# Optimization experiments

Hardware: AMD Instinct MI355X
Metric: run time of the kernel (lower is better)

The kernel has to match this reference:

```python
import jax, jax.numpy as jnp
import numpy as np

B, N, C = 8, 1024, 768
H = 12
DH = C // H  # 64
FF = 3072
EPS = 1e-5


def _layer_norm(x, gamma, beta):
    mu = jnp.mean(x, axis=-1, keepdims=True)
    var = jnp.mean(jnp.square(x - mu), axis=-1, keepdims=True)
    return (x - mu) * jax.lax.rsqrt(var + EPS) * gamma + beta


def setup_inputs() -> dict:
    key = jax.random.key(0)
    ks = jax.random.split(key, 16)
    s_in = 1.0 / np.sqrt(C)
    s_ff = 1.0 / np.sqrt(FF)
    return {
        "x": jax.random.normal(ks[0], (B, N, C), dtype=jnp.float32),
        "Wq": jax.random.uniform(ks[1], (C, C), jnp.float32, -s_in, s_in),
        "bq": jax.random.uniform(ks[2], (C,), jnp.float32, -s_in, s_in),
        "Wk": jax.random.uniform(ks[3], (C, C), jnp.float32, -s_in, s_in),
        "bk": jax.random.uniform(ks[4], (C,), jnp.float32, -s_in, s_in),
        "Wv": jax.random.uniform(ks[5], (C, C), jnp.float32, -s_in, s_in),
        "bv": jax.random.uniform(ks[6], (C,), jnp.float32, -s_in, s_in),
        "Wo": jax.random.uniform(ks[7], (C, C), jnp.float32, -s_in, s_in),
        "bo": jax.random.uniform(ks[8], (C,), jnp.float32, -s_in, s_in),
        "g1": jnp.ones((C,), jnp.float32),
        "b1": jnp.zeros((C,), jnp.float32),
        "g2": jnp.ones((C,), jnp.float32),
        "b2": jnp.zeros((C,), jnp.float32),
        "W1": jax.random.uniform(ks[9], (C, FF), jnp.float32, -s_in, s_in),
        "bf1": jax.random.uniform(ks[10], (FF,), jnp.float32, -s_in, s_in),
        "W2": jax.random.uniform(ks[11], (FF, C), jnp.float32, -s_ff, s_ff),
        "bf2": jax.random.uniform(ks[12], (C,), jnp.float32, -s_ff, s_ff),
    }


def reference(x, Wq, bq, Wk, bk, Wv, bv, Wo, bo, g1, b1, g2, b2, W1, bf1, W2, bf2):
    # Pre-norm attention block
    xn = _layer_norm(x, g1, b1)
    q = (xn @ Wq + bq).reshape(B, N, H, DH)
    k = (xn @ Wk + bk).reshape(B, N, H, DH)
    v = (xn @ Wv + bv).reshape(B, N, H, DH)
    scores = jnp.einsum("bqhd,bkhd->bhqk", q, k) / np.sqrt(DH)  # [B,H,N,N]
    attn = jax.nn.softmax(scores, axis=-1)
    z = jnp.einsum("bhqk,bkhd->bqhd", attn, v).reshape(B, N, C)
    attn_out = z @ Wo + bo
    b = x + attn_out  # dropout is identity (p=0 / eval)
    # Pre-norm MLP block
    bn = _layer_norm(b, g2, b2)
    h = jax.nn.relu(bn @ W1 + bf1)
    y = b + (h @ W2 + bf2)
    return y
```

## Files before the change

### kernel.cpp

```cpp
#include <hip/hip_runtime.h>
#include <hip/hip_bf16.h>

#define BDIM 8
#define SEQ  1024
#define CH   768
#define NHD  12
#define DHD  64
#define FFD  3072
#define MR   (BDIM*SEQ)

typedef __attribute__((ext_vector_type(8))) short bf16x8;
typedef __attribute__((ext_vector_type(4))) float f32x4;
typedef unsigned int   u32;
typedef unsigned short u16;

__device__ __forceinline__ u16 f2bfu(float x) {
  __hip_bfloat16 h = __float2bfloat16(x);
  return *reinterpret_cast<u16*>(&h);
}

__device__ __forceinline__ void glds16(const void* g, void* l) {
  __builtin_amdgcn_global_load_lds(
      (const __attribute__((address_space(1))) u32*)g,
      (__attribute__((address_space(3))) u32*)l, 16, 0, 0);
}

__global__ __launch_bounds__(256) void k_transpose_all(
    const float* __restrict__ Wq, const float* __restrict__ Wk,
    const float* __restrict__ Wv, const float* __restrict__ Wo,
    const float* __restrict__ W1, const float* __restrict__ W2,
    u16* __restrict__ ws, const float* __restrict__ bq,
    const float* __restrict__ bk, const float* __restrict__ bv,
    float* __restrict__ bdst) {
  __shared__ float tile[32][33];
  int b = blockIdx.x;
  if (b >= 6912) {
    int i = (b - 6912) * 256 + threadIdx.x;
    if (i < 3 * CH)
      bdst[i] = i < CH ? bq[i] : (i < 2 * CH ? bk[i - CH] : bv[i - 2 * CH]);
    return;
  }
  int id, tb;
  if (b < 2304)      { id = b / 576; tb = b % 576; }
  else if (b < 4608) { id = 4;       tb = b - 2304; }
  else               { id = 5;       tb = b - 4608; }
  const float* src;
  u16* dst;
  int K, Nc;
  switch (id) {
    case 0: src = Wq; dst = ws;                      K = CH;  Nc = CH;  break;
    case 1: src = Wk; dst = ws + (size_t)CH*CH;      K = CH;  Nc = CH;  break;
    case 2: src = Wv; dst = ws + (size_t)2*CH*CH;    K = CH;  Nc = CH;  break;
    case 3: src = Wo; dst = ws + (size_t)3*CH*CH;    K = CH;  Nc = CH;  break;
    case 4: src = W1; dst = ws + (size_t)4*CH*CH;    K = CH;  Nc = FFD; break;
    default:src = W2; dst = ws + (size_t)4*CH*CH + (size_t)CH*FFD;
                                                     K = FFD; Nc = CH;  break;
  }
  int tilesx = Nc >> 5;
  int bx = (tb % tilesx) * 32;
  int by = (tb / tilesx) * 32;
  int tx = threadIdx.x & 31, ty = threadIdx.x >> 5;
#pragma unroll
  for (int j = 0; j < 32; j += 8)
    tile[ty + j][tx] = src[(size_t)(by + ty + j) * Nc + bx + tx];
  __syncthreads();
#pragma unroll
  for (int j = 0; j < 32; j += 8)
    dst[(size_t)(bx + ty + j) * K + by + tx] = f2bfu(tile[tx][ty + j]);
}

__global__ __launch_bounds__(256) void k_layernorm_bf16(
    const float* __restrict__ src, const float* __restrict__ gamma,
    const float* __restrict__ beta, u16* __restrict__ dst) {
  int row  = blockIdx.x * 4 + (threadIdx.x >> 6);
  int lane = threadIdx.x & 63;
  const float4* p4 = (const float4*)(src + (size_t)row * CH);
  float4 v[3];
  float s = 0.f, s2 = 0.f;
#pragma unroll
  for (int k = 0; k < 3; k++) {
    v[k] = p4[lane + k * 64];
    s  += v[k].x + v[k].y + v[k].z + v[k].w;
    s2 += v[k].x * v[k].x + v[k].y * v[k].y + v[k].z * v[k].z + v[k].w * v[k].w;
  }
#pragma unroll
  for (int m = 1; m < 64; m <<= 1) {
    s  += __shfl_xor(s,  m, 64);
    s2 += __shfl_xor(s2, m, 64);
  }
  float mean = s * (1.f / CH);
  float var  = s2 * (1.f / CH) - mean * mean;
  float rs   = rsqrtf(var + 1e-5f);
  u16* drow = dst + (size_t)row * CH;
#pragma unroll
  for (int k = 0; k < 3; k++) {
    int col = lane * 4 + k * 256;
    float4 gq = ((const float4*)gamma)[lane + k * 64];
    float4 bq = ((const float4*)beta )[lane + k * 64];
    u32 lo = (u32)f2bfu((v[k].x - mean) * rs * gq.x + bq.x) |
             ((u32)f2bfu((v[k].y - mean) * rs * gq.y + bq.y) << 16);
    u32 hi = (u32)f2bfu((v[k].z - mean) * rs * gq.z + bq.z) |
             ((u32)f2bfu((v[k].w - mean) * rs * gq.w + bq.w) << 16);
    uint2 w; w.x = lo; w.y = hi;
    *(uint2*)(drow + col) = w;
  }
}

enum { EPI_QKV = 0, EPI_RESID = 1, EPI_RELU = 2 };

template <int EPI>
__device__ __forceinline__ void gemm_epi(const f32x4& a, int row0, int col,
                                         float bval, const float* resid,
                                         void* outp, int Nmat) {
  if constexpr (EPI == EPI_QKV) {
    int sel = col / CH;
    int c = col - sel * CH;
    int h = c >> 6, d = c & 63;
    int bb = row0 >> 10, nn0 = row0 & (SEQ - 1);
    if (sel == 2) {
      union { uint2 u; u16 h4[4]; } pk;
#pragma unroll
      for (int r = 0; r < 4; r++) pk.h4[r] = f2bfu(a[r] + bval);
      *(uint2*)&((u16*)outp)[(size_t)2 * MR * CH +
                             (((size_t)(bb * NHD + h)) * DHD + d) * SEQ + nn0] =
          pk.u;
    } else {
#pragma unroll
      for (int r = 0; r < 4; r++)
        ((u16*)outp)[(size_t)sel * MR * CH +
                     (((size_t)(bb * NHD + h)) * SEQ + nn0 + r) * DHD + d] =
            f2bfu(a[r] + bval);
    }
  } else if constexpr (EPI == EPI_RESID) {
#pragma unroll
    for (int r = 0; r < 4; r++) {
      size_t idx = (size_t)(row0 + r) * Nmat + col;
      ((float*)outp)[idx] = a[r] + bval + resid[idx];
    }
  } else {
#pragma unroll
    for (int r = 0; r < 4; r++) {
      float val = a[r] + bval;
      ((u16*)outp)[(size_t)(row0 + r) * Nmat + col] =
          f2bfu(val > 0.f ? val : 0.f);
    }
  }
}

template <int EPI, int TM = 128>
__global__ __launch_bounds__(256, 2) void k_gemm(
    const u16* __restrict__ A, const u16* __restrict__ Bt,
    const float* __restrict__ bias, const float* __restrict__ resid,
    void* __restrict__ outp, int K, int Nmat) {
  __shared__ u16 As[2][TM * 32];
  __shared__ u16 Bs[2][128 * 32];
  constexpr int MF = TM / 32;
  int tid = threadIdx.x;
  int bm = blockIdx.x, bn = blockIdx.y;
  int lane = tid & 63, wid = tid >> 6;
  int wr = (wid >> 1) * (TM / 2), wc = (wid & 1) * 64;
  int lrow = lane & 15, g = lane >> 4;

  const u16* Abase = A + (size_t)(bm * TM) * K;
  const u16* Bbase = Bt + (size_t)(bn * 128) * K;

  auto stage = [&](int buf, int k0) {
#pragma unroll
    for (int r = 0; r < TM / 64; r++) {
      int c = tid + r * 256;
      int row = c >> 2;
      int scol = ((c & 3) ^ ((row >> 1) & 3)) * 8;
      glds16(Abase + (size_t)row * K + k0 + scol, &As[buf][c * 8]);
    }
#pragma unroll
    for (int r = 0; r < 2; r++) {
      int c = tid + r * 256;
      int row = c >> 2;
      int scol = ((c & 3) ^ ((row >> 1) & 3)) * 8;
      glds16(Bbase + (size_t)row * K + k0 + scol, &Bs[buf][c * 8]);
    }
  };

  int xsl = (g ^ ((lrow >> 1) & 3)) * 8;

  f32x4 acc[MF][4];
#pragma unroll
  for (int m = 0; m < MF; m++)
#pragma unroll
    for (int n = 0; n < 4; n++) acc[m][n] = {0.f, 0.f, 0.f, 0.f};

  int nk = K >> 5;
  stage(0, 0);
  for (int kt = 0; kt < nk; ++kt) {
    int buf = kt & 1;
    __syncthreads();
    if (kt + 1 < nk) stage(buf ^ 1, (kt + 1) << 5);
    bf16x8 af[MF], bfr[4];
#pragma unroll
    for (int m = 0; m < MF; m++)
      af[m] = *(const bf16x8*)&As[buf][(wr + m * 16 + lrow) * 32 + xsl];
#pragma unroll
    for (int n = 0; n < 4; n++)
      bfr[n] = *(const bf16x8*)&Bs[buf][(wc + n * 16 + lrow) * 32 + xsl];
    __builtin_amdgcn_s_setprio(1);
#pragma unroll
    for (int m = 0; m < MF; m++)
#pragma unroll
      for (int n = 0; n < 4; n++)
        acc[m][n] = __builtin_amdgcn_mfma_f32_16x16x32_bf16(af[m], bfr[n],
                                                            acc[m][n], 0, 0, 0);
    __builtin_amdgcn_s_setprio(0);
  }

#pragma unroll
  for (int m = 0; m < MF; m++) {
    int row0 = bm * TM + wr + m * 16 + g * 4;
#pragma unroll
    for (int n = 0; n < 4; n++) {
      int col = bn * 128 + wc + n * 16 + lrow;
      gemm_epi<EPI>(acc[m][n], row0, col, bias[col], resid, outp, Nmat);
    }
  }
}

template <int EPI>
__global__ __launch_bounds__(256, 2) void k_gemmk64(
    const u16* __restrict__ A, const u16* __restrict__ Bt,
    const float* __restrict__ bias, const float* __restrict__ resid,
    void* __restrict__ outp, int K, int Nmat) {
  __shared__ u16 As[2][64 * 64];
  __shared__ u16 Bs[2][128 * 64];
  int tid = threadIdx.x;
  int bm = blockIdx.x, bn = blockIdx.y;
  int lane = tid & 63, wid = tid >> 6;
  int wr = (wid >> 1) * 32, wc = (wid & 1) * 64;
  int lrow = lane & 15, g = lane >> 4;

  const u16* Abase = A + (size_t)(bm * 64) * K;
  const u16* Bbase = Bt + (size_t)(bn * 128) * K;

  auto stage = [&](int buf, int k0) {
#pragma unroll
    for (int r = 0; r < 2; r++) {
      int u = tid + r * 256;
      int row = u >> 3, slot = u & 7;
      glds16(Abase + (size_t)row * K + k0 + ((slot ^ (row & 7)) << 3),
             &As[buf][u * 8]);
    }
#pragma unroll
    for (int r = 0; r < 4; r++) {
      int u = tid + r * 256;
      int row = u >> 3, slot = u & 7;
      glds16(Bbase + (size_t)row * K + k0 + ((slot ^ (row & 7)) << 3),
             &Bs[buf][u * 8]);
    }
  };

  int sx = lrow & 7;
  int x0 = (g ^ sx) * 8;
  int x1 = ((4 + g) ^ sx) * 8;

  f32x4 acc[2][4];
#pragma unroll
  for (int m = 0; m < 2; m++)
#pragma unroll
    for (int n = 0; n < 4; n++) acc[m][n] = {0.f, 0.f, 0.f, 0.f};

  int nk = K >> 6;
  stage(0, 0);
  for (int kt = 0; kt < nk; ++kt) {
    int buf = kt & 1;
    __syncthreads();
    if (kt + 1 < nk) stage(buf ^ 1, (kt + 1) << 6);
#pragma unroll
    for (int ks = 0; ks < 2; ks++) {
      int xs = ks ? x1 : x0;
      bf16x8 af[2], bfr[4];
#pragma unroll
      for (int m = 0; m < 2; m++)
        af[m] = *(const bf16x8*)&As[buf][(wr + m * 16 + lrow) * 64 + xs];
#pragma unroll
      for (int n = 0; n < 4; n++)
        bfr[n] = *(const bf16x8*)&Bs[buf][(wc + n * 16 + lrow) * 64 + xs];
      __builtin_amdgcn_s_setprio(1);
#pragma unroll
      for (int m = 0; m < 2; m++)
#pragma unroll
        for (int n = 0; n < 4; n++)
          acc[m][n] = __builtin_amdgcn_mfma_f32_16x16x32_bf16(
              af[m], bfr[n], acc[m][n], 0, 0, 0);
      __builtin_amdgcn_s_setprio(0);
    }
  }

#pragma unroll
  for (int m = 0; m < 2; m++) {
    int row0 = bm * 64 + wr + m * 16 + g * 4;
#pragma unroll
    for (int n = 0; n < 4; n++) {
      int col = bn * 128 + wc + n * 16 + lrow;
      gemm_epi<EPI>(acc[m][n], row0, col, bias[col], resid, outp, Nmat);
    }
  }
}

__global__ __launch_bounds__(512, 4) void k_attn(
    const u16* __restrict__ Q, const u16* __restrict__ Kk,
    const u16* __restrict__ Vt, u16* __restrict__ Z) {
  __shared__ u16 Ks[2][64 * 64];
  __shared__ u16 Vs[2][64 * 64];
  __shared__ u32 Psu[8][64 * 9];
  int tid = threadIdx.x, lane = tid & 63, wid = tid >> 6;
  int lrow = lane & 15, g = lane >> 4;
  int id  = blockIdx.x;
  int nid = (id & 7) * 96 + (id >> 3);
  int bh = nid >> 3;
  int qtile = (nid & 7) * 128;
  size_t base = (size_t)bh * SEQ * DHD;
  int bb = bh / NHD, hh = bh % NHD;
  int qrow0 = qtile + wid * 16;

  bf16x8 qf[2];
#pragma unroll
  for (int ks = 0; ks < 2; ks++)
    qf[ks] = *(const bf16x8*)(Q + base + (size_t)(qrow0 + lrow) * DHD +
                              ks * 32 + g * 8);

  f32x4 accO[4];
  float mrun = -1e30f, lrun = 0.f;
#pragma unroll
  for (int n = 0; n < 4; n++) accO[n] = {0.f, 0.f, 0.f, 0.f};

  int srow = tid >> 3;
  int swz  = (((tid & 7) * 16) ^ ((srow & 7) << 4)) >> 1;
  const u16* kg0 = Kk + base + (size_t)srow * DHD + swz;
  const u16* vg0 = Vt + base + (size_t)srow * SEQ + swz;

  auto stageKV = [&](int buf, int t) {
    glds16(kg0 + (size_t)t * 64 * DHD, &Ks[buf][tid * 8]);
    glds16(vg0 + t * 64,               &Vs[buf][tid * 8]);
  };

  int rc0 = ((g * 16)      ^ ((lrow & 7) << 4)) >> 1;
  int rc1 = ((64 + g * 16) ^ ((lrow & 7) << 4)) >> 1;

  stageKV(0, 0);
  for (int t = 0; t < 16; ++t) {
    int buf = t & 1;
    __syncthreads();
    if (t + 1 < 16) stageKV(buf ^ 1, t + 1);

    f32x4 sacc[4];
    __builtin_amdgcn_s_setprio(1);
#pragma unroll
    for (int n = 0; n < 4; n++) {
      bf16x8 kf0 = *(const bf16x8*)&Ks[buf][(n * 16 + lrow) * 64 + rc0];
      bf16x8 kf1 = *(const bf16x8*)&Ks[buf][(n * 16 + lrow) * 64 + rc1];
      sacc[n] = {0.f, 0.f, 0.f, 0.f};
      sacc[n] = __builtin_amdgcn_mfma_f32_16x16x32_bf16(kf0, qf[0], sacc[n], 0, 0, 0);
      sacc[n] = __builtin_amdgcn_mfma_f32_16x16x32_bf16(kf1, qf[1], sacc[n], 0, 0, 0);
    }
    __builtin_amdgcn_s_setprio(0);

    float mx = fmaxf(fmaxf(fmaxf(sacc[0][0], sacc[0][1]),
                           fmaxf(sacc[0][2], sacc[0][3])),
                     fmaxf(fmaxf(sacc[1][0], sacc[1][1]),
                           fmaxf(sacc[1][2], sacc[1][3])));
    mx = fmaxf(mx, fmaxf(fmaxf(fmaxf(sacc[2][0], sacc[2][1]),
                               fmaxf(sacc[2][2], sacc[2][3])),
                         fmaxf(fmaxf(sacc[3][0], sacc[3][1]),
                               fmaxf(sacc[3][2], sacc[3][3]))));
    mx *= 0.125f;
    mx = fmaxf(mx, __shfl_xor(mx, 16, 64));
    mx = fmaxf(mx, __shfl_xor(mx, 32, 64));

    if (__all(mx <= mrun + 8.f)) {
      float psum = 0.f;
#pragma unroll
      for (int n = 0; n < 4; n++)
#pragma unroll
        for (int r = 0; r < 4; r++) {
          float p = __expf(sacc[n][r] * 0.125f - mrun);
          sacc[n][r] = p;
          psum += p;
        }
      psum += __shfl_xor(psum, 16, 64);
      psum += __shfl_xor(psum, 32, 64);
      lrun += psum;
    } else {
      float mnew = fmaxf(mrun, mx);
      float alpha = __expf(mrun - mnew);
      float psum = 0.f;
#pragma unroll
      for (int n = 0; n < 4; n++)
#pragma unroll
        for (int r = 0; r < 4; r++) {
          float p = __expf(sacc[n][r] * 0.125f - mnew);
          sacc[n][r] = p;
          psum += p;
        }
      psum += __shfl_xor(psum, 16, 64);
      psum += __shfl_xor(psum, 32, 64);
      lrun = lrun * alpha + psum;
      mrun = mnew;
#pragma unroll
      for (int r = 0; r < 4; r++) {
        float ar = __shfl(alpha, (lane & 48) | (g * 4 + r), 64);
#pragma unroll
        for (int n = 0; n < 4; n++) accO[n][r] *= ar;
      }
    }

#pragma unroll
    for (int n = 0; n < 4; n++) {
      u32 lo = (u32)f2bfu(sacc[n][0]) | ((u32)f2bfu(sacc[n][1]) << 16);
      u32 hi = (u32)f2bfu(sacc[n][2]) | ((u32)f2bfu(sacc[n][3]) << 16);
      Psu[wid][lane * 9 + 2 * n]     = lo;
      Psu[wid][lane * 9 + 2 * n + 1] = hi;
    }

    int laneA = lrow + ((g & 1) << 5);
    int laneB = laneA + 16;
    int nsel = g >> 1;
    __builtin_amdgcn_s_setprio(1);
#pragma unroll
    for (int ks = 0; ks < 2; ks++) {
      int nks = 2 * ks + nsel;
      union { bf16x8 v; u32 w[4]; } pk;
      pk.w[0] = Psu[wid][laneA * 9 + 2 * nks];
      pk.w[1] = Psu[wid][laneA * 9 + 2 * nks + 1];
      pk.w[2] = Psu[wid][laneB * 9 + 2 * nks];
      pk.w[3] = Psu[wid][laneB * 9 + 2 * nks + 1];
      int rc = ks ? rc1 : rc0;
#pragma unroll
      for (int n = 0; n < 4; n++) {
        bf16x8 vf = *(const bf16x8*)&Vs[buf][(n * 16 + lrow) * 64 + rc];
        accO[n] = __builtin_amdgcn_mfma_f32_16x16x32_bf16(pk.v, vf,
                                                          accO[n], 0, 0, 0);
      }
    }
    __builtin_amdgcn_s_setprio(0);
  }

#pragma unroll
  for (int r = 0; r < 4; r++) {
    float lr = __shfl(lrun, (lane & 48) | (g * 4 + r), 64);
    float inv = 1.f / lr;
    int qrow = qrow0 + g * 4 + r;
#pragma unroll
    for (int n = 0; n < 4; n++) {
      int d = n * 16 + lrow;
      Z[((size_t)(bb * SEQ + qrow)) * CH + hh * DHD + d] =
          f2bfu(accO[n][r] * inv);
    }
  }
}

extern "C" void kernel_launch(void* const* d_in, const int* in_sizes, int n_in,
                              void* d_out, int out_size, void* d_ws,
                              size_t ws_size, hipStream_t stream) {
  (void)in_sizes; (void)n_in; (void)out_size; (void)ws_size;
  const float* x   = (const float*)d_in[0];
  const float* Wq  = (const float*)d_in[1];
  const float* bq  = (const float*)d_in[2];
  const float* Wk  = (const float*)d_in[3];
  const float* bk  = (const float*)d_in[4];
  const float* Wv  = (const float*)d_in[5];
  const float* bv  = (const float*)d_in[6];
  const float* Wo  = (const float*)d_in[7];
  const float* bo  = (const float*)d_in[8];
  const float* g1  = (const float*)d_in[9];
  const float* b1  = (const float*)d_in[10];
  const float* g2  = (const float*)d_in[11];
  const float* b2  = (const float*)d_in[12];
  const float* W1  = (const float*)d_in[13];
  const float* bf1 = (const float*)d_in[14];
  const float* W2  = (const float*)d_in[15];
  const float* bf2 = (const float*)d_in[16];

  u16* wsu  = (u16*)d_ws;
  u16* wq_t = wsu;
  u16* wo_t = wq_t + (size_t)3 * CH * CH;
  u16* w1_t = wo_t + (size_t)CH * CH;
  u16* w2_t = w1_t + (size_t)CH * FFD;
  u16* xn   = w2_t + (size_t)CH * FFD;
  u16* qb   = xn + (size_t)MR * CH;
  u16* zb   = qb + (size_t)3 * MR * CH;
  float* bres = (float*)(zb + (size_t)MR * CH);
  u16* hb   = qb;
  float* bqkv = (float*)d_out;

  dim3 blk(256);
  k_transpose_all<<<6921, blk, 0, stream>>>(Wq, Wk, Wv, Wo, W1, W2, wsu,
                                            bq, bk, bv, bqkv);

  k_layernorm_bf16<<<2048, blk, 0, stream>>>(x, g1, b1, xn);
  k_gemm<EPI_QKV, 128><<<dim3(64, 18), blk, 0, stream>>>(
      xn, wq_t, bqkv, nullptr, qb, CH, 3 * CH);
  k_attn<<<768, dim3(512), 0, stream>>>(qb, qb + (size_t)MR * CH,
                                        qb + (size_t)2 * MR * CH, zb);
  k_gemm<EPI_RESID, 64><<<dim3(128, 6), blk, 0, stream>>>(
      zb, wo_t, bo, x, bres, CH, CH);
  k_layernorm_bf16<<<2048, blk, 0, stream>>>(bres, g2, b2, xn);
  k_gemm<EPI_RELU, 128><<<dim3(64, 24), blk, 0, stream>>>(
      xn, w1_t, bf1, nullptr, hb, CH, FFD);
  k_gemmk64<EPI_RESID><<<dim3(128, 6), blk, 0, stream>>>(
      hb, w2_t, bf2, bres, (float*)d_out, FFD, CH);
}
```

Before: 248.6 us.

## Use K64 GEMM kernel for all projections and streamline attention softmax

```diff
diff --git a/kernel.cpp b/kernel.cpp
--- a/kernel.cpp
+++ b/kernel.cpp
@@ -17,6 +17,12 @@
 __device__ __forceinline__ u16 f2bfu(float x) {
   __hip_bfloat16 h = __float2bfloat16(x);
   return *reinterpret_cast<u16*>(&h);
+}
+
+__device__ __forceinline__ u32 pk2(float a, float b) {
+  u32 ua = __float_as_uint(a) + 0x8000u;
+  u32 ub = __float_as_uint(b) + 0x8000u;
+  return (ub & 0xFFFF0000u) | (ua >> 16);
 }
 
 __device__ __forceinline__ void glds16(const void* g, void* l) {
@@ -147,82 +153,6 @@
   }
 }
 
-template <int EPI, int TM = 128>
-__global__ __launch_bounds__(256, 2) void k_gemm(
-    const u16* __restrict__ A, const u16* __restrict__ Bt,
-    const float* __restrict__ bias, const float* __restrict__ resid,
-    void* __restrict__ outp, int K, int Nmat) {
-  __shared__ u16 As[2][TM * 32];
-  __shared__ u16 Bs[2][128 * 32];
-  constexpr int MF = TM / 32;
-  int tid = threadIdx.x;
-  int bm = blockIdx.x, bn = blockIdx.y;
-  int lane = tid & 63, wid = tid >> 6;
-  int wr = (wid >> 1) * (TM / 2), wc = (wid & 1) * 64;
-  int lrow = lane & 15, g = lane >> 4;
-
-  const u16* Abase = A + (size_t)(bm * TM) * K;
-  const u16* Bbase = Bt + (size_t)(bn * 128) * K;
-
-  auto stage = [&](int buf, int k0) {
-#pragma unroll
-    for (int r = 0; r < TM / 64; r++) {
-      int c = tid + r * 256;
-      int row = c >> 2;
-      int scol = ((c & 3) ^ ((row >> 1) & 3)) * 8;
-      glds16(Abase + (size_t)row * K + k0 + scol, &As[buf][c * 8]);
-    }
-#pragma unroll
-    for (int r = 0; r < 2; r++) {
-      int c = tid + r * 256;
-      int row = c >> 2;
-      int scol = ((c & 3) ^ ((row >> 1) & 3)) * 8;
-      glds16(Bbase + (size_t)row * K + k0 + scol, &Bs[buf][c * 8]);
-    }
-  };
-
-  int xsl = (g ^ ((lrow >> 1) & 3)) * 8;
-
-  f32x4 acc[MF][4];
-#pragma unroll
-  for (int m = 0; m < MF; m++)
-#pragma unroll
-    for (int n = 0; n < 4; n++) acc[m][n] = {0.f, 0.f, 0.f, 0.f};
-
-  int nk = K >> 5;
-  stage(0, 0);
-  for (int kt = 0; kt < nk; ++kt) {
-    int buf = kt & 1;
-    __syncthreads();
-    if (kt + 1 < nk) stage(buf ^ 1, (kt + 1) << 5);
-    bf16x8 af[MF], bfr[4];
-#pragma unroll
-    for (int m = 0; m < MF; m++)
-      af[m] = *(const bf16x8*)&As[buf][(wr + m * 16 + lrow) * 32 + xsl];
-#pragma unroll
-    for (int n = 0; n < 4; n++)
-      bfr[n] = *(const bf16x8*)&Bs[buf][(wc + n * 16 + lrow) * 32 + xsl];
-    __builtin_amdgcn_s_setprio(1);
-#pragma unroll
-    for (int m = 0; m < MF; m++)
-#pragma unroll
-      for (int n = 0; n < 4; n++)
-        acc[m][n] = __builtin_amdgcn_mfma_f32_16x16x32_bf16(af[m], bfr[n],
-                                                            acc[m][n], 0, 0, 0);
-    __builtin_amdgcn_s_setprio(0);
-  }
-
-#pragma unroll
-  for (int m = 0; m < MF; m++) {
-    int row0 = bm * TM + wr + m * 16 + g * 4;
-#pragma unroll
-    for (int n = 0; n < 4; n++) {
-      int col = bn * 128 + wc + n * 16 + lrow;
-      gemm_epi<EPI>(acc[m][n], row0, col, bias[col], resid, outp, Nmat);
-    }
-  }
-}
-
 template <int EPI>
 __global__ __launch_bounds__(256, 2) void k_gemmk64(
     const u16* __restrict__ A, const u16* __restrict__ Bt,
@@ -310,6 +240,7 @@
   __shared__ u16 Ks[2][64 * 64];
   __shared__ u16 Vs[2][64 * 64];
   __shared__ u32 Psu[8][64 * 9];
+  const float S2 = 0.18033688f;
   int tid = threadIdx.x, lane = tid & 63, wid = tid >> 6;
   int lrow = lane & 15, g = lane >> 4;
   int id  = blockIdx.x;
@@ -370,17 +301,17 @@
                                fmaxf(sacc[2][2], sacc[2][3])),
                          fmaxf(fmaxf(sacc[3][0], sacc[3][1]),
                                fmaxf(sacc[3][2], sacc[3][3]))));
-    mx *= 0.125f;
+    mx *= S2;
     mx = fmaxf(mx, __shfl_xor(mx, 16, 64));
     mx = fmaxf(mx, __shfl_xor(mx, 32, 64));
 
-    if (__all(mx <= mrun + 8.f)) {
+    if (__all(mx <= mrun + 11.5f)) {
       float psum = 0.f;
 #pragma unroll
       for (int n = 0; n < 4; n++)
 #pragma unroll
         for (int r = 0; r < 4; r++) {
-          float p = __expf(sacc[n][r] * 0.125f - mrun);
+          float p = exp2f(fmaf(sacc[n][r], S2, -mrun));
           sacc[n][r] = p;
           psum += p;
         }
@@ -389,13 +320,13 @@
       lrun += psum;
     } else {
       float mnew = fmaxf(mrun, mx);
-      float alpha = __expf(mrun - mnew);
+      float alpha = exp2f(mrun - mnew);
       float psum = 0.f;
 #pragma unroll
       for (int n = 0; n < 4; n++)
 #pragma unroll
         for (int r = 0; r < 4; r++) {
-          float p = __expf(sacc[n][r] * 0.125f - mnew);
+          float p = exp2f(fmaf(sacc[n][r], S2, -mnew));
           sacc[n][r] = p;
           psum += p;
         }
@@ -413,10 +344,8 @@
 
 #pragma unroll
     for (int n = 0; n < 4; n++) {
-      u32 lo = (u32)f2bfu(sacc[n][0]) | ((u32)f2bfu(sacc[n][1]) << 16);
-      u32 hi = (u32)f2bfu(sacc[n][2]) | ((u32)f2bfu(sacc[n][3]) << 16);
-      Psu[wid][lane * 9 + 2 * n]     = lo;
-      Psu[wid][lane * 9 + 2 * n + 1] = hi;
+      Psu[wid][lane * 9 + 2 * n]     = pk2(sacc[n][0], sacc[n][1]);
+      Psu[wid][lane * 9 + 2 * n + 1] = pk2(sacc[n][2], sacc[n][3]);
     }
 
     int laneA = lrow + ((g & 1) << 5);
@@ -495,14 +424,14 @@
                                             bq, bk, bv, bqkv);
 
   k_layernorm_bf16<<<2048, blk, 0, stream>>>(x, g1, b1, xn);
-  k_gemm<EPI_QKV, 128><<<dim3(64, 18), blk, 0, stream>>>(
+  k_gemmk64<EPI_QKV><<<dim3(128, 18), blk, 0, stream>>>(
       xn, wq_t, bqkv, nullptr, qb, CH, 3 * CH);
   k_attn<<<768, dim3(512), 0, stream>>>(qb, qb + (size_t)MR * CH,
                                         qb + (size_t)2 * MR * CH, zb);
-  k_gemm<EPI_RESID, 64><<<dim3(128, 6), blk, 0, stream>>>(
+  k_gemmk64<EPI_RESID><<<dim3(128, 6), blk, 0, stream>>>(
       zb, wo_t, bo, x, bres, CH, CH);
   k_layernorm_bf16<<<2048, blk, 0, stream>>>(bres, g2, b2, xn);
-  k_gemm<EPI_RELU, 128><<<dim3(64, 24), blk, 0, stream>>>(
+  k_gemmk64<EPI_RELU><<<dim3(128, 24), blk, 0, stream>>>(
       xn, w1_t, bf1, nullptr, hb, CH, FFD);
   k_gemmk64<EPI_RESID><<<dim3(128, 6), blk, 0, stream>>>(
       hb, w2_t, bf2, bres, (float*)d_out, FFD, CH);
```

Result: no change. 244.4 us (-1.7%).
